# Kernel optimization log

Hardware: AMD Instinct MI355X
Metric: run time of the kernel (lower is better)

## Reference

```python
import jax, jax.numpy as jnp
import numpy as np

jax.config.update("jax_enable_x64", True)

B, T, D, L, H = 128, 256, 64, 64, 256   # batch, time steps, phys dim, latent dim, hidden width
P, DT = 4, 1.0                          # num_pred_steps, delta_t


def _mlp(x, ws, bs):
    # Conv1D(kernel_size=1) stack == per-timestep dense; relu hidden, linear output
    for i, (W, b) in enumerate(zip(ws, bs)):
        x = x @ W + b
        if i < len(ws) - 1:
            x = jax.nn.relu(x)
    return x


def setup_inputs() -> dict:
    key = jax.random.key(0)
    ks = jax.random.split(key, 9)

    def glorot(k, fi, fo):
        return jax.random.normal(k, (fi, fo), jnp.float64) * np.sqrt(2.0 / (fi + fo))

    inp = {"x": jax.random.normal(ks[0], (B, T, D), jnp.float64)}
    enc_dims = [(D, H), (H, H), (H, H), (H, L)]
    dec_dims = [(L, H), (H, H), (H, H), (H, D)]
    for i, (fi, fo) in enumerate(enc_dims):
        inp[f"enc_w{i}"] = glorot(ks[1 + i], fi, fo)
        inp[f"enc_b{i}"] = jnp.zeros((fo,), jnp.float64)
    for i, (fi, fo) in enumerate(dec_dims):
        inp[f"dec_w{i}"] = glorot(ks[5 + i], fi, fo)
        inp[f"dec_b{i}"] = jnp.zeros((fo,), jnp.float64)
    return inp


def _edmd(y, x):
    # y: [B, L, T] latent trajectories, x: [B, D, T] physical trajectories (D == L)
    y_m, y_p = y[:, :, :-1], y[:, :, 1:]
    # full_matrices=True followed by slicing to r=min(L,T-1)=L cols == reduced SVD
    U, S, Vh = jnp.linalg.svd(y_m, full_matrices=False)
    V = jnp.swapaxes(Vh, -1, -2)
    pinv = (V / S[:, None, :]) @ jnp.swapaxes(U, -1, -2)   # V @ diag(1/S) @ U^H
    K = y_p @ pinv                                         # [B, L, L]
    evals, modes = jnp.linalg.eig(K)                       # complex128
    k_evals = jnp.log(evals) / DT                          # [B, L]
    k_efuns = jnp.linalg.solve(modes, x.astype(modes.dtype))  # [B, L, T]
    xint = k_efuns[:, :, -1:]                              # [B, L, 1]

    # repeated squaring of diag eigenvalue matrix, one matvec per prediction step
    def step(e, _):
        yp = (modes @ (e[:, :, None] * xint))[..., 0]      # [B, L]
        return e * e, yp

    _, ys = jax.lax.scan(step, k_evals * k_evals, None, length=P)
    y_pred = jnp.transpose(ys, (1, 0, 2))                  # [B, P, L]
    return k_efuns, k_evals, modes, y_pred


def reference(x, enc_w0, enc_b0, enc_w1, enc_b1, enc_w2, enc_b2, enc_w3, enc_b3,
              dec_w0, dec_b0, dec_w1, dec_b1, dec_w2, dec_b2, dec_w3, dec_b3):
    ews = [enc_w0, enc_w1, enc_w2, enc_w3]
    ebs = [enc_b0, enc_b1, enc_b2, enc_b3]
    dws = [dec_w0, dec_w1, dec_w2, dec_w3]
    dbs = [dec_b0, dec_b1, dec_b2, dec_b3]

    y = _mlp(x, ews, ebs)        # [B, T, L]
    x_ae = _mlp(y, dws, dbs)     # [B, T, D]

    yt = jnp.swapaxes(y, 1, 2)   # [B, L, T]
    xt = jnp.swapaxes(x, 1, 2)   # [B, D, T]
    k_efuns, k_evals, k_modes, y_adv = _edmd(yt, xt)
    y_adv_real = jnp.real(y_adv)
    y_adv_imag = jnp.imag(y_adv)
    x_adv = _mlp(y_adv_real, dws, dbs)  # [B, P, D]
    return y, x_ae, x_adv, y_adv_real, y_adv_imag, k_evals, k_efuns, k_modes
```

## Files before the change

kernel.cpp:

```cpp
#include <hip/hip_runtime.h>
#include <hip/hip_bf16.h>

#define NB 128
#define NT 256
#define ND 64
#define NL 64
#define NH 256
#define NP 4

__device__ double g_ws[3932160];

static __device__ __forceinline__ double dlapy2_(double x, double y) {
  double ax = fabs(x), ay = fabs(y);
  double w = ax > ay ? ax : ay;
  double z = ax > ay ? ay : ax;
  if (z == 0.0) return w;
  double r = z / w;
  return w * sqrt(1.0 + r * r);
}
static __device__ __forceinline__ double sgn1_(double x) { return copysign(1.0, x); }
static __device__ __forceinline__ void cdiv_(double ar, double ai, double br, double bi,
                                             double& cr, double& ci) {
  if (fabs(br) >= fabs(bi)) {
    double r = bi / br, den = br + r * bi;
    cr = (ar + ai * r) / den;
    ci = (ai - ar * r) / den;
  } else {
    double r = br / bi, den = bi + r * br;
    cr = (ar * r + ai) / den;
    ci = (ai * r - ar) / den;
  }
}
static __device__ __forceinline__ void fwg(float* out, long long ofs, long long lim,
                                           double v) {
  if (ofs >= 0 && ofs < lim) out[ofs] = (float)v;
}
static __device__ __forceinline__ double wsum_(double v) {
  for (int o = 32; o > 0; o >>= 1) v += __shfl_xor(v, o, 64);
  return v;
}
static __device__ __forceinline__ double wmax_(double v) {
  for (int o = 32; o > 0; o >>= 1) v = fmax(v, __shfl_xor(v, o, 64));
  return v;
}
static __device__ __forceinline__ void wbar() {
  asm volatile("" ::: "memory");
  __builtin_amdgcn_wave_barrier();
  asm volatile("" ::: "memory");
}

static __device__ void dlanv2_(double& a, double& b, double& c, double& d,
                               double& rt1r, double& rt1i, double& rt2r, double& rt2i,
                               double& cs, double& sn) {
  const double eps = 2.2204460492503131e-16;
  if (c == 0.0) {
    cs = 1.0; sn = 0.0;
  } else if (b == 0.0) {
    cs = 0.0; sn = 1.0;
    double temp = d; d = a; a = temp;
    b = -c; c = 0.0;
  } else if ((a - d) == 0.0 && sgn1_(b) != sgn1_(c)) {
    cs = 1.0; sn = 0.0;
  } else {
    double temp = a - d;
    double p = 0.5 * temp;
    double bcmax = fmax(fabs(b), fabs(c));
    double bcmis = fmin(fabs(b), fabs(c)) * sgn1_(b) * sgn1_(c);
    double scale = fmax(fabs(p), bcmax);
    double z = (p / scale) * p + (bcmax / scale) * bcmis;
    if (z >= 4.0 * eps) {
      z = p + copysign(sqrt(scale) * sqrt(z), p);
      a = d + z;
      d = d - (bcmax / z) * bcmis;
      double tau = dlapy2_(c, z);
      cs = z / tau; sn = c / tau;
      b = b - c; c = 0.0;
    } else {
      double sigma = b + c;
      double tau = dlapy2_(sigma, temp);
      cs = sqrt(0.5 * (1.0 + fabs(sigma) / tau));
      sn = -(p / (tau * cs)) * sgn1_(sigma);
      double aa = a * cs + b * sn, bb = -a * sn + b * cs;
      double cc = c * cs + d * sn, dd = -c * sn + d * cs;
      a = aa * cs + cc * sn; b = bb * cs + dd * sn;
      c = -aa * sn + cc * cs; d = -bb * sn + dd * cs;
      temp = 0.5 * (a + d);
      a = temp; d = temp;
      if (c != 0.0) {
        if (b != 0.0) {
          if (sgn1_(b) == sgn1_(c)) {
            double sab = sqrt(fabs(b)), sac = sqrt(fabs(c));
            double p2 = copysign(sab * sac, c);
            double tau2 = 1.0 / sqrt(fabs(b + c));
            a = temp + p2; d = temp - p2;
            b = b - c; c = 0.0;
            double cs1 = sab * tau2, sn1 = sac * tau2;
            double t0 = cs * cs1 - sn * sn1;
            sn = cs * sn1 + sn * cs1;
            cs = t0;
          }
        } else {
          b = -c; c = 0.0;
          double t0 = cs; cs = -sn; sn = t0;
        }
      }
    }
  }
  rt1r = a; rt2r = d;
  if (c == 0.0) { rt1i = 0.0; rt2i = 0.0; }
  else { rt1i = sqrt(fabs(b)) * sqrt(fabs(c)); rt2i = -rt1i; }
}

__global__ __launch_bounds__(256) void enc_kernel(
    const float* __restrict__ x,
    const float* __restrict__ EW0, const float* __restrict__ EB0,
    const float* __restrict__ EW1, const float* __restrict__ EB1,
    const float* __restrict__ EW2, const float* __restrict__ EB2,
    const float* __restrict__ EW3, const float* __restrict__ EB3,
    float* __restrict__ out_y, double* __restrict__ y64, long long lim)
{
  const int tid = threadIdx.x;
  const long long tok0 = (long long)blockIdx.x * 8;
  __shared__ double xin[8][64];
  __shared__ double h0[8][256];
  __shared__ double h1[8][256];
  for (int idx = tid; idx < 512; idx += 256) {
    int tk = idx >> 6, f2 = idx & 63;
    xin[tk][f2] = (double)x[(tok0 + tk) * 64 + f2];
  }
  __syncthreads();
  {
    int j = tid; double acc[8]; double bj = (double)EB0[j];
    for (int tk = 0; tk < 8; ++tk) acc[tk] = bj;
#pragma unroll 8
    for (int i2 = 0; i2 < 64; ++i2) {
      double w = (double)EW0[i2 * 256 + j];
      for (int tk = 0; tk < 8; ++tk) acc[tk] += xin[tk][i2] * w;
    }
    for (int tk = 0; tk < 8; ++tk) h0[tk][j] = fmax(acc[tk], 0.0);
  }
  __syncthreads();
  {
    int j = tid; double acc[8]; double bj = (double)EB1[j];
    for (int tk = 0; tk < 8; ++tk) acc[tk] = bj;
#pragma unroll 4
    for (int i2 = 0; i2 < 256; ++i2) {
      double w = (double)EW1[i2 * 256 + j];
      for (int tk = 0; tk < 8; ++tk) acc[tk] += h0[tk][i2] * w;
    }
    for (int tk = 0; tk < 8; ++tk) h1[tk][j] = fmax(acc[tk], 0.0);
  }
  __syncthreads();
  {
    int j = tid; double acc[8]; double bj = (double)EB2[j];
    for (int tk = 0; tk < 8; ++tk) acc[tk] = bj;
#pragma unroll 4
    for (int i2 = 0; i2 < 256; ++i2) {
      double w = (double)EW2[i2 * 256 + j];
      for (int tk = 0; tk < 8; ++tk) acc[tk] += h1[tk][i2] * w;
    }
    for (int tk = 0; tk < 8; ++tk) h0[tk][j] = fmax(acc[tk], 0.0);
  }
  __syncthreads();
  {
    int j = tid & 63;
    int tg = tid >> 6;
    double acc0 = (double)EB3[j], acc1 = acc0;
#pragma unroll 4
    for (int i2 = 0; i2 < 256; ++i2) {
      double w = (double)EW3[i2 * 64 + j];
      acc0 += h0[tg * 2][i2] * w;
      acc1 += h0[tg * 2 + 1][i2] * w;
    }
    for (int u = 0; u < 2; ++u) {
      int tk = tg * 2 + u;
      double a = (u == 0) ? acc0 : acc1;
      long long gl = (tok0 + tk) * 64 + j;
      fwg(out_y, gl, lim, a);
      y64[gl] = a;
    }
  }
}

__global__ __launch_bounds__(256) void dec4_kernel(
    const double* __restrict__ inp, long long ntok,
    const float* __restrict__ W0, const float* __restrict__ B0,
    const float* __restrict__ W1, const float* __restrict__ B1,
    const float* __restrict__ W2, const float* __restrict__ B2,
    const float* __restrict__ W3, const float* __restrict__ B3,
    float* __restrict__ outb, long long lim)
{
  const int tid = threadIdx.x;
  const long long tok0 = (long long)blockIdx.x * 8;
  __shared__ double xin[8][64];
  __shared__ double h0[8][256];
  __shared__ double h1[8][256];
  for (int idx = tid; idx < 512; idx += 256) {
    int tk = idx >> 6, f2 = idx & 63;
    long long gl = (tok0 + tk) * 64 + f2;
    xin[tk][f2] = (tok0 + tk < ntok) ? inp[gl] : 0.0;
  }
  __syncthreads();
  {
    int j = tid; double acc[8]; double bj = (double)B0[j];
    for (int tk = 0; tk < 8; ++tk) acc[tk] = bj;
#pragma unroll 8
    for (int i2 = 0; i2 < 64; ++i2) {
      double w = (double)W0[i2 * 256 + j];
      for (int tk = 0; tk < 8; ++tk) acc[tk] += xin[tk][i2] * w;
    }
    for (int tk = 0; tk < 8; ++tk) h0[tk][j] = fmax(acc[tk], 0.0);
  }
  __syncthreads();
  {
    int j = tid; double acc[8]; double bj = (double)B1[j];
    for (int tk = 0; tk < 8; ++tk) acc[tk] = bj;
#pragma unroll 4
    for (int i2 = 0; i2 < 256; ++i2) {
      double w = (double)W1[i2 * 256 + j];
      for (int tk = 0; tk < 8; ++tk) acc[tk] += h0[tk][i2] * w;
    }
    for (int tk = 0; tk < 8; ++tk) h1[tk][j] = fmax(acc[tk], 0.0);
  }
  __syncthreads();
  {
    int j = tid; double acc[8]; double bj = (double)B2[j];
    for (int tk = 0; tk < 8; ++tk) acc[tk] = bj;
#pragma unroll 4
    for (int i2 = 0; i2 < 256; ++i2) {
      double w = (double)W2[i2 * 256 + j];
      for (int tk = 0; tk < 8; ++tk) acc[tk] += h1[tk][i2] * w;
    }
    for (int tk = 0; tk < 8; ++tk) h0[tk][j] = fmax(acc[tk], 0.0);
  }
  __syncthreads();
  {
    int j = tid & 63;
    int tg = tid >> 6;
    double acc0 = (double)B3[j], acc1 = acc0;
#pragma unroll 4
    for (int i2 = 0; i2 < 256; ++i2) {
      double w = (double)W3[i2 * 64 + j];
      acc0 += h0[tg * 2][i2] * w;
      acc1 += h0[tg * 2 + 1][i2] * w;
    }
    for (int u = 0; u < 2; ++u) {
      long long tok = tok0 + tg * 2 + u;
      if (tok < ntok) fwg(outb, tok * 64 + j, lim, (u == 0) ? acc0 : acc1);
    }
  }
}

__global__ __launch_bounds__(256) void buildGA_kernel(const double* __restrict__ y64,
                                                      double* __restrict__ G,
                                                      double* __restrict__ A)
{
  int b = blockIdx.x, tid = threadIdx.x;
  __shared__ double ybuf[65][64];
  const double* yb = y64 + (size_t)b * NT * 64;
  double g[16], a[16];
  for (int s = 0; s < 16; ++s) { g[s] = 0.0; a[s] = 0.0; }
  for (int c0 = 0; c0 < 255; c0 += 64) {
    int nrow = (256 - c0 < 65) ? (256 - c0) : 65;
    for (int idx = tid; idx < nrow * 64; idx += 256) {
      int rr = idx >> 6, f2 = idx & 63;
      ybuf[rr][f2] = yb[(size_t)(c0 + rr) * 64 + f2];
    }
    __syncthreads();
    int tmax = (254 - c0 < 63) ? (254 - c0) : 63;
    for (int s = 0; s < 16; ++s) {
      int id = s * 256 + tid;
      int i2 = id >> 6, j2 = id & 63;
      double gg = g[s], aa = a[s];
      for (int tt = 0; tt <= tmax; ++tt) {
        double yj = ybuf[tt][j2];
        gg += ybuf[tt][i2] * yj;
        aa += ybuf[tt + 1][i2] * yj;
      }
      g[s] = gg; a[s] = aa;
    }
    __syncthreads();
  }
  for (int s = 0; s < 16; ++s) {
    int id = s * 256 + tid;
    G[(size_t)b * 4096 + id] = g[s];
    A[(size_t)b * 4096 + id] = a[s];
  }
}

__global__ __launch_bounds__(64) void cholsolve_kernel(const double* __restrict__ G,
                                                       const double* __restrict__ A,
                                                       double* __restrict__ Km)
{
  int b = blockIdx.x, t = threadIdx.x;
  __shared__ double C[64][65];
  __shared__ double X[64][65];
  const double* Gb = G + (size_t)b * 4096;
  const double* Ab = A + (size_t)b * 4096;
  for (int r = 0; r < 64; ++r) C[r][t] = Gb[r * 64 + t];
  for (int i2 = 0; i2 < 64; ++i2) X[i2][t] = Ab[t * 64 + i2];
  __syncthreads();
  for (int k = 0; k < 64; ++k) {
    double s = C[k][k];
    for (int m2 = 0; m2 < k; ++m2) s -= C[k][m2] * C[k][m2];
    double ckk = sqrt(fmax(s, 1e-300));
    wbar();
    if (t == k) C[k][k] = ckk;
    if (t > k) {
      double v = C[t][k];
      for (int m2 = 0; m2 < k; ++m2) v -= C[t][m2] * C[k][m2];
      C[t][k] = v / ckk;
    }
    wbar();
  }
  for (int i2 = 0; i2 < 64; ++i2) {
    double v = X[i2][t];
    for (int m2 = 0; m2 < i2; ++m2) v -= C[i2][m2] * X[m2][t];
    X[i2][t] = v / C[i2][i2];
  }
  for (int i2 = 63; i2 >= 0; --i2) {
    double v = X[i2][t];
    for (int m2 = i2 + 1; m2 < 64; ++m2) v -= C[m2][i2] * X[m2][t];
    X[i2][t] = v / C[i2][i2];
  }
  wbar();
  for (int i2 = 0; i2 < 64; ++i2)
    Km[(size_t)b * 4096 + (size_t)t * 64 + i2] = X[i2][t];
}

__global__ __launch_bounds__(64) void eig_dec_kernel(
    const double* __restrict__ Kmat,
    double* __restrict__ modes_re, double* __restrict__ modes_im,
    double* __restrict__ klog,
    float* __restrict__ out, long long o_kevals, long long o_kmodes,
    int cplx, long long lim,
    const double* __restrict__ y64,
    const float* __restrict__ DW0, const float* __restrict__ DB0,
    const float* __restrict__ DW1, const float* __restrict__ DB1,
    const float* __restrict__ DW2, const float* __restrict__ DB2,
    const float* __restrict__ DW3, const float* __restrict__ DB3,
    float* __restrict__ out_xae)
{
  const int t = threadIdx.x;
  __shared__ __align__(16) double smem[8704];

  if (blockIdx.x >= NB) {
    const int blk = blockIdx.x - NB;
    const long long tok0 = (long long)blk * 8;
    float (*fx)[64] = (float (*)[64])(smem);
    float (*fh0)[256] = (float (*)[256])(smem + 256);
    float (*fh1)[256] = (float (*)[256])(smem + 1280);
    for (int idx = t; idx < 512; idx += 64) {
      int tk = idx >> 6, f2 = idx & 63;
      fx[tk][f2] = (float)y64[(tok0 + tk) * 64 + f2];
    }
    __syncthreads();
    float acc[4][8];
    for (int s = 0; s < 4; ++s) {
      float bj = DB0[t + 64 * s];
      for (int tk = 0; tk < 8; ++tk) acc[s][tk] = bj;
    }
#pragma unroll 4
    for (int i = 0; i < 64; ++i) {
      float xv[8];
      for (int tk = 0; tk < 8; ++tk) xv[tk] = fx[tk][i];
      for (int s = 0; s < 4; ++s) {
        float w = DW0[i * 256 + t + 64 * s];
        for (int tk = 0; tk < 8; ++tk) acc[s][tk] += xv[tk] * w;
      }
    }
    for (int s = 0; s < 4; ++s)
      for (int tk = 0; tk < 8; ++tk) fh0[tk][t + 64 * s] = fmaxf(acc[s][tk], 0.0f);
    __syncthreads();
    for (int s = 0; s < 4; ++s) {
      float bj = DB1[t + 64 * s];
      for (int tk = 0; tk < 8; ++tk) acc[s][tk] = bj;
    }
#pragma unroll 2
    for (int i = 0; i < 256; ++i) {
      float xv[8];
      for (int tk = 0; tk < 8; ++tk) xv[tk] = fh0[tk][i];
      for (int s = 0; s < 4; ++s) {
        float w = DW1[i * 256 + t + 64 * s];
        for (int tk = 0; tk < 8; ++tk) acc[s][tk] += xv[tk] * w;
      }
    }
    for (int s = 0; s < 4; ++s)
      for (int tk = 0; tk < 8; ++tk) fh1[tk][t + 64 * s] = fmaxf(acc[s][tk], 0.0f);
    __syncthreads();
    for (int s = 0; s < 4; ++s) {
      float bj = DB2[t + 64 * s];
      for (int tk = 0; tk < 8; ++tk) acc[s][tk] = bj;
    }
#pragma unroll 2
    for (int i = 0; i < 256; ++i) {
      float xv[8];
      for (int tk = 0; tk < 8; ++tk) xv[tk] = fh1[tk][i];
      for (int s = 0; s < 4; ++s) {
        float w = DW2[i * 256 + t + 64 * s];
        for (int tk = 0; tk < 8; ++tk) acc[s][tk] += xv[tk] * w;
      }
    }
    for (int s = 0; s < 4; ++s)
      for (int tk = 0; tk < 8; ++tk) fh0[tk][t + 64 * s] = fmaxf(acc[s][tk], 0.0f);
    __syncthreads();
    float a4[8];
    float bj3 = DB3[t];
    for (int tk = 0; tk < 8; ++tk) a4[tk] = bj3;
#pragma unroll 2
    for (int i = 0; i < 256; ++i) {
      float w = DW3[i * 64 + t];
      for (int tk = 0; tk < 8; ++tk) a4[tk] += fh0[tk][i] * w;
    }
    for (int tk = 0; tk < 8; ++tk)
      fwg(out_xae, (tok0 + tk) * 64 + t, lim, (double)a4[tk]);
    return;
  }

  const int b = blockIdx.x;
  double (*Hs)[65] = (double (*)[65])smem;
  double (*Zs)[65] = (double (*)[65])(smem + 4160);
  double* wr = smem + 8320;
  double* wi = wr + 64;
  double* bscale = wi + 64;
  double* tau = bscale + 64;
  double* xr = tau + 64;
  double* xi = xr + 64;
  double* mre = modes_re + (size_t)b * 4096;
  double* mim = modes_im + (size_t)b * 4096;

  const double ulp = 2.2204460492503131e-16;
  const double safmin = 2.2250738585072014e-308;

  for (int r = 0; r < 64; ++r) Hs[r][t] = Kmat[(size_t)b * 4096 + r * 64 + t];
  bscale[t] = 1.0;
  __syncthreads();

  {
    const double sclfac = 2.0, factor = 0.95;
    const double sfmin1 = safmin / ulp;
    const double sfmax1 = 1.0 / sfmin1;
    const double sfmin2 = sfmin1 * sclfac;
    const double sfmax2 = 1.0 / sfmin2;
    for (int sweep = 0; sweep < 64; ++sweep) {
      bool noconv = false;
      for (int i = 0; i < 64; ++i) {
        double colv = fabs(Hs[t][i]);
        double rowv = fabs(Hs[i][t]);
        double c = wsum_((t == i) ? 0.0 : colv);
        double r = wsum_((t == i) ? 0.0 : rowv);
        double ca = wmax_(colv);
        double ra = wmax_(rowv);
        if (c == 0.0 || r == 0.0) continue;
        double g = r / sclfac, f = 1.0, s = c + r;
        while (c < g) {
          if (fmax(fmax(f, c), ca) >= sfmax2 || fmin(fmin(r, g), ra) <= sfmin2) break;
          f *= sclfac; c *= sclfac; ca *= sclfac;
          r /= sclfac; g /= sclfac; ra /= sclfac;
        }
        g = c / sclfac;
        while (g >= r) {
          if (fmax(r, ra) >= sfmax2 || fmin(fmin(fmin(f, c), g), ca) <= sfmin2) break;
          f /= sclfac; c /= sclfac; g /= sclfac; ca /= sclfac;
          r *= sclfac; ra *= sclfac;
        }
        if (c + r >= factor * s) continue;
        double bsi = bscale[i];
        if (f < 1.0 && bsi < 1.0) { if (f * bsi <= sfmin1) continue; }
        if (f > 1.0 && bsi > 1.0) { if (bsi >= sfmax1 / f) continue; }
        double gi = 1.0 / f;
        Hs[i][t] *= gi;
        Hs[t][i] *= f;
        if (t == 0) bscale[i] = bsi * f;
        noconv = true;
        wbar();
      }
      if (!noconv) break;
    }
    wbar();
  }

  for (int i = 0; i < 62; ++i) {
    double alpha = Hs[i + 1][i];
    double contrib = (t >= i + 2) ? Hs[t][i] * Hs[t][i] : 0.0;
    double ss = wsum_(contrib);
    double taui, beta;
    if (ss == 0.0) {
      taui = 0.0; beta = alpha;
    } else {
      beta = -copysign(sqrt(alpha * alpha + ss), alpha);
      taui = (beta - alpha) / beta;
      double sc = 1.0 / (alpha - beta);
      if (t >= i + 2) Hs[t][i] *= sc;
    }
    if (t == 0) { tau[i] = taui; Hs[i + 1][i] = beta; }
    wbar();
    if (taui != 0.0) {
      {
        double sum = Hs[t][i + 1];
        for (int k = i + 2; k < 64; ++k) sum += Hs[t][k] * Hs[k][i];
        sum *= taui;
        Hs[t][i + 1] -= sum;
        for (int k = i + 2; k < 64; ++k) Hs[t][k] -= sum * Hs[k][i];
      }
      wbar();
      if (t >= i + 1) {
        double sum = Hs[i + 1][t];
        for (int k = i + 2; k < 64; ++k) sum += Hs[k][i] * Hs[k][t];
        sum *= taui;
        Hs[i + 1][t] -= sum;
        for (int k = i + 2; k < 64; ++k) Hs[k][t] -= sum * Hs[k][i];
      }
      wbar();
    }
  }

  {
    for (int r = 0; r < 64; ++r) Zs[t][r] = (r == t) ? 1.0 : 0.0;
    for (int i = 61; i >= 0; --i) {
      double taui = tau[i];
      if (taui != 0.0) {
        double sum = Zs[t][i + 1];
        for (int k = i + 2; k < 64; ++k) sum += Hs[k][i] * Zs[t][k];
        sum *= taui;
        Zs[t][i + 1] -= sum;
        for (int k = i + 2; k < 64; ++k) Zs[t][k] -= sum * Hs[k][i];
      }
    }
  }
  wbar();
  for (int r = t + 2; r < 64; ++r) Hs[r][t] = 0.0;
  __syncthreads();

  {
    const int lo = 0, hi = 63;
    const double dat1 = 0.75, dat2 = -0.4375;
    const int kexsh = 10;
    const double smlnum = safmin * (64.0 / ulp);
    int I = hi;
    int kdefl = 0;
    while (I >= lo) {
      int L = lo;
      bool done = false;
      const int itmax = 30 * 64;
      for (int its = 0; its <= itmax; ++its) {
        int k;
        {
          bool pred = false;
          int kl = t;
          if (kl > L && kl <= I) {
            double sub = fabs(Hs[kl][kl - 1]);
            if (sub <= smlnum) pred = true;
            else {
              double tst = fabs(Hs[kl - 1][kl - 1]) + fabs(Hs[kl][kl]);
              if (tst == 0.0) {
                if (kl - 2 >= lo) tst += fabs(Hs[kl - 1][kl - 2]);
                if (kl + 1 <= hi) tst += fabs(Hs[kl + 1][kl]);
              }
              if (sub <= ulp * tst) {
                double h12a = fabs(Hs[kl - 1][kl]);
                double ab = fmax(sub, h12a), ba = fmin(sub, h12a);
                double hkk = fabs(Hs[kl][kl]);
                double dif = fabs(Hs[kl - 1][kl - 1] - Hs[kl][kl]);
                double aa = fmax(hkk, dif), bb2 = fmin(hkk, dif);
                double s = aa + ab;
                if (ba * (ab / s) <= fmax(smlnum, ulp * (bb2 * (aa / s)))) pred = true;
              }
            }
          }
          unsigned long long msk = __ballot(pred);
          k = msk ? (63 - __builtin_clzll(msk)) : L;
        }
        L = k;
        if (L > lo) { if (t == 0) Hs[L][L - 1] = 0.0; }
        wbar();
        if (L >= I - 1) { done = true; break; }
        kdefl++;
        double h11, h12, h21, h22;
        if (kdefl % (2 * kexsh) == 0) {
          double s = dat1 * (fabs(Hs[I][I - 1]) + fabs(Hs[I - 1][I - 2]));
          h11 = dat2 * s + Hs[I][I]; h12 = s; h21 = s; h22 = h11;
        } else if (kdefl % kexsh == 0) {
          double s = dat1 * (fabs(Hs[L + 1][L]) + fabs(Hs[L + 2][L + 1]));
          h11 = dat2 * s + Hs[L][L]; h12 = s; h21 = s; h22 = h11;
        } else {
          h11 = Hs[I - 1][I - 1]; h21 = Hs[I][I - 1];
          h12 = Hs[I - 1][I];     h22 = Hs[I][I];
        }
        double rt1r, rt1i, rt2r, rt2i;
        {
          double s = fabs(h11) + fabs(h12) + fabs(h21) + fabs(h22);
          if (s == 0.0) { rt1r = rt1i = rt2r = rt2i = 0.0; }
          else {
            double a_ = h11 / s, c_ = h21 / s, b_ = h12 / s, d_ = h22 / s;
            double tr = a_ + d_;
            double det = (a_ - d_) * (a_ - d_) * 0.25 + b_ * c_;
            if (det >= 0.0) {
              double rtdisc = sqrt(det);
              double r1 = tr * 0.5 + rtdisc;
              double r2 = tr * 0.5 - rtdisc;
              double pick = (fabs(r1 - d_) <= fabs(r2 - d_)) ? r1 : r2;
              rt1r = pick * s; rt2r = rt1r; rt1i = 0.0; rt2i = 0.0;
            } else {
              rt1r = tr * 0.5 * s; rt2r = rt1r;
              rt1i = sqrt(-det) * s; rt2i = -rt1i;
            }
          }
        }
        int m; double v0, v1, v2;
        {
          double w0 = 0.0, w1 = 0.0, w2 = 0.0;
          bool ok = false;
          int mm = t;
          if (mm >= L && mm <= I - 2) {
            double h21s = Hs[mm + 1][mm];
            double s = fabs(Hs[mm][mm] - rt2r) + fabs(rt2i) + fabs(h21s);
            h21s = Hs[mm + 1][mm] / s;
            w0 = h21s * Hs[mm][mm + 1] + (Hs[mm][mm] - rt1r) * ((Hs[mm][mm] - rt2r) / s)
                 - rt1i * (rt2i / s);
            w1 = h21s * (Hs[mm][mm] + Hs[mm + 1][mm + 1] - rt1r - rt2r);
            w2 = h21s * Hs[mm + 2][mm + 1];
            double s2 = fabs(w0) + fabs(w1) + fabs(w2);
            w0 /= s2; w1 /= s2; w2 /= s2;
            if (mm == L) ok = true;
            else ok = (fabs(Hs[mm][mm - 1]) * (fabs(w1) + fabs(w2)) <=
                       ulp * fabs(w0) *
                           (fabs(Hs[mm - 1][mm - 1]) + fabs(Hs[mm][mm]) +
                            fabs(Hs[mm + 1][mm + 1])));
          }
          unsigned long long msk = __ballot(ok);
          m = 63 - __builtin_clzll(msk);
          v0 = __shfl(w0, m); v1 = __shfl(w1, m); v2 = __shfl(w2, m);
        }
        double c0 = 0.0, c1 = 0.0, c2 = 0.0;
        double zc0 = 0.0, zc1 = 0.0;
        for (int kk = m; kk <= I - 1; ++kk) {
          int nr = (3 < I - kk + 1) ? 3 : (I - kk + 1);
          double a0 = Hs[kk][t];
          double a1 = Hs[kk + 1][t];
          double a2 = (nr == 3) ? Hs[kk + 2][t] : 0.0;
          double z0, z1;
          if (kk > m) { z0 = zc0; z1 = zc1; }
          else { z0 = Zs[kk][t]; z1 = Zs[kk + 1][t]; }
          double z2 = (nr == 3) ? Zs[kk + 2][t] : 0.0;
          double u0, u1, u2 = 0.0;
          if (kk > m) { u0 = c0; u1 = c1; u2 = (nr == 3) ? c2 : 0.0; }
          else        { u0 = v0; u1 = v1; u2 = (nr == 3) ? v2 : 0.0; }
          double t1;
          {
            double xn2 = u1 * u1 + u2 * u2;
            if (xn2 == 0.0) t1 = 0.0;
            else {
              double beta = -copysign(sqrt(u0 * u0 + xn2), u0);
              t1 = (beta - u0) / beta;
              double sc = 1.0 / (u0 - beta);
              u1 *= sc; u2 *= sc;
              u0 = beta;
            }
          }
          double t2 = t1 * u1, t3 = t1 * u2;
          if (t >= kk) {
            double sum = a0 + u1 * a1 + u2 * a2;
            Hs[kk][t] = a0 - sum * t1;
            Hs[kk + 1][t] = a1 - sum * t2;
            if (nr == 3) Hs[kk + 2][t] = a2 - sum * t3;
          }
          if (t == 0) {
            if (kk > m) {
              Hs[kk][kk - 1] = u0;
              Hs[kk + 1][kk - 1] = 0.0;
              if (kk < I - 1) Hs[kk + 2][kk - 1] = 0.0;
            } else if (m > L) {
              Hs[kk][kk - 1] *= (1.0 - t1);
            }
          }
          wbar();
          int rmax = (kk + 3 < I) ? kk + 3 : I;
          double nv0 = 0.0;
          if (t <= rmax) {
            double b0 = Hs[t][kk], b1 = Hs[t][kk + 1];
            double b2 = (nr == 3) ? Hs[t][kk + 2] : 0.0;
            double sB = b0 + u1 * b1 + u2 * b2;
            nv0 = b0 - sB * t1;
            Hs[t][kk] = nv0;
            Hs[t][kk + 1] = b1 - sB * t2;
            if (nr == 3) Hs[t][kk + 2] = b2 - sB * t3;
          }
          {
            double sZ = z0 + u1 * z1 + u2 * z2;
            Zs[kk][t] = z0 - sZ * t1;
            zc0 = z1 - sZ * t2;
            Zs[kk + 1][t] = zc0;
            if (nr == 3) {
              zc1 = z2 - sZ * t3;
              Zs[kk + 2][t] = zc1;
            }
          }
          int s1 = (kk + 1 < 64) ? kk + 1 : 63;
          int s2 = (kk + 2 < 64) ? kk + 2 : 63;
          int s3 = (kk + 3 < 64) ? kk + 3 : 63;
          c0 = __shfl(nv0, s1, 64);
          c1 = __shfl(nv0, s2, 64);
          c2 = __shfl(nv0, s3, 64);
          wbar();
        }
      }
      if (!done) {
        wbar();
        if (t == 0) {
          for (int r = lo; r <= I; ++r) { wr[r] = Hs[r][r]; wi[r] = 0.0; }
        }
        wbar();
        I = lo - 1;
        kdefl = 0;
        continue;
      }
      if (L == I) {
        if (t == 0) { wr[I] = Hs[I][I]; wi[I] = 0.0; }
        wbar();
      } else {
        double a_ = Hs[I - 1][I - 1], b_ = Hs[I - 1][I];
        double c_ = Hs[I][I - 1],     d_ = Hs[I][I];
        double r1r, r1i, r2r, r2i, cs, sn;
        dlanv2_(a_, b_, c_, d_, r1r, r1i, r2r, r2i, cs, sn);
        wbar();
        if (t == 0) {
          Hs[I - 1][I - 1] = a_; Hs[I - 1][I] = b_;
          Hs[I][I - 1] = c_;     Hs[I][I] = d_;
          wr[I - 1] = r1r; wi[I - 1] = r1i;
          wr[I] = r2r;     wi[I] = r2i;
        }
        wbar();
        if (t > I) {
          double x = Hs[I - 1][t], y = Hs[I][t];
          Hs[I - 1][t] = cs * x + sn * y;
          Hs[I][t] = cs * y - sn * x;
        }
        if (t < I - 1) {
          double x = Hs[t][I - 1], y = Hs[t][I];
          Hs[t][I - 1] = cs * x + sn * y;
          Hs[t][I] = cs * y - sn * x;
        }
        {
          double x = Zs[I - 1][t], y = Zs[I][t];
          Zs[I - 1][t] = cs * x + sn * y;
          Zs[I][t] = cs * y - sn * x;
        }
        wbar();
      }
      kdefl = 0;
      I = L - 1;
    }
  }
  __syncthreads();

  const double smln = safmin * (64.0 / ulp);
  int ki = 63;
  while (ki >= 0) {
    wbar();
    bool pair = (ki > 0) && (Hs[ki][ki - 1] != 0.0);
    if (!pair) {
      double lam = wr[ki];
      double smin = fmax(ulp * fabs(lam), smln);
      xr[t] = (t < ki) ? -Hs[t][ki] : ((t == ki) ? 1.0 : 0.0);
      wbar();
      int j = ki - 1;
      while (j >= 0) {
        bool blk2 = (j > 0) && (Hs[j][j - 1] != 0.0);
        if (!blk2) {
          double den = Hs[j][j] - lam;
          if (fabs(den) < smin) den = smin;
          double xj = xr[j] / den;
          if (t == j) xr[j] = xj;
          else if (t < j) xr[t] -= xj * Hs[t][j];
          wbar();
          j -= 1;
        } else {
          double t11 = Hs[j - 1][j - 1] - lam, t12 = Hs[j - 1][j];
          double t21 = Hs[j][j - 1], t22 = Hs[j][j] - lam;
          double det = t11 * t22 - t12 * t21;
          if (fabs(det) < smin * smin) det = copysign(smin * smin, (det == 0.0) ? 1.0 : det);
          double b1 = xr[j - 1], b2 = xr[j];
          double x1 = (b1 * t22 - t12 * b2) / det;
          double x2 = (t11 * b2 - t21 * b1) / det;
          if (t == j - 1) xr[j - 1] = x1;
          else if (t == j) xr[j] = x2;
          else if (t < j - 1) xr[t] -= x1 * Hs[t][j - 1] + x2 * Hs[t][j];
          wbar();
          j -= 2;
        }
      }
      double acc = 0.0;
      for (int k2 = 0; k2 <= ki; ++k2) acc += Zs[k2][t] * xr[k2];
      acc *= bscale[t];
      double nn = wsum_(acc * acc);
      double scl = 1.0 / sqrt(nn);
      mre[t * 64 + ki] = acc * scl;
      mim[t * 64 + ki] = 0.0;
      ki -= 1;
    } else {
      double wre = Hs[ki][ki];
      double wim = sqrt(fabs(Hs[ki][ki - 1])) * sqrt(fabs(Hs[ki - 1][ki]));
      double smin = fmax(ulp * (fabs(wre) + wim), smln);
      double seed_r_km1, seed_i_k;
      if (fabs(Hs[ki - 1][ki]) >= fabs(Hs[ki][ki - 1])) {
        seed_r_km1 = 1.0;
        seed_i_k = wim / Hs[ki - 1][ki];
      } else {
        seed_r_km1 = -wim / Hs[ki][ki - 1];
        seed_i_k = 1.0;
      }
      if (t < ki - 1) {
        xr[t] = -seed_r_km1 * Hs[t][ki - 1];
        xi[t] = -seed_i_k * Hs[t][ki];
      } else if (t == ki - 1) { xr[t] = seed_r_km1; xi[t] = 0.0; }
      else if (t == ki) { xr[t] = 0.0; xi[t] = seed_i_k; }
      else { xr[t] = 0.0; xi[t] = 0.0; }
      wbar();
      int j = ki - 2;
      while (j >= 0) {
        bool blk2 = (j > 0) && (Hs[j][j - 1] != 0.0);
        if (!blk2) {
          double dr = Hs[j][j] - wre, di = -wim;
          if (fabs(dr) + fabs(di) < smin) { dr = smin; di = 0.0; }
          double xjr, xji;
          cdiv_(xr[j], xi[j], dr, di, xjr, xji);
          if (t == j) { xr[j] = xjr; xi[j] = xji; }
          else if (t < j) {
            xr[t] -= xjr * Hs[t][j];
            xi[t] -= xji * Hs[t][j];
          }
          wbar();
          j -= 1;
        } else {
          double t11 = Hs[j - 1][j - 1] - wre, t12 = Hs[j - 1][j];
          double t21 = Hs[j][j - 1], t22 = Hs[j][j] - wre;
          double detr = t11 * t22 - wim * wim - t12 * t21;
          double deti = -wim * (t11 + t22);
          double b1r = xr[j - 1], b1i = xi[j - 1];
          double b2r = xr[j], b2i = xi[j];
          double n1r = b1r * t22 + b1i * wim - t12 * b2r;
          double n1i = b1i * t22 - b1r * wim - t12 * b2i;
          double n2r = t11 * b2r + b2i * wim - t21 * b1r;
          double n2i = t11 * b2i - b2r * wim - t21 * b1i;
          double x1r, x1i, x2r, x2i;
          cdiv_(n1r, n1i, detr, deti, x1r, x1i);
          cdiv_(n2r, n2i, detr, deti, x2r, x2i);
          if (t == j - 1) { xr[t] = x1r; xi[t] = x1i; }
          else if (t == j) { xr[t] = x2r; xi[t] = x2i; }
          else if (t < j - 1) {
            xr[t] -= x1r * Hs[t][j - 1] + x2r * Hs[t][j];
            xi[t] -= x1i * Hs[t][j - 1] + x2i * Hs[t][j];
          }
          wbar();
          j -= 2;
        }
      }
      double ar = 0.0, ai = 0.0;
      for (int k2 = 0; k2 <= ki; ++k2) {
        double z = Zs[k2][t];
        ar += z * xr[k2];
        ai += z * xi[k2];
      }
      ar *= bscale[t]; ai *= bscale[t];
      double n2a = wsum_(ar * ar), n2b = wsum_(ai * ai);
      double scl = 1.0 / dlapy2_(sqrt(n2a), sqrt(n2b));
      double vr0 = ar * scl, vi0 = ai * scl;
      double mm = vr0 * vr0 + vi0 * vi0;
      double mmax = wmax_(mm);
      unsigned long long msk = __ballot(mm == mmax);
      int kmx = __ffsll((unsigned long long)msk) - 1;
      double f = __shfl(vr0, kmx), g = __shfl(vi0, kmx);
      double cs_, sn_;
      if (g == 0.0) { cs_ = 1.0; sn_ = 0.0; }
      else if (f == 0.0) { cs_ = 0.0; sn_ = sgn1_(g); }
      else {
        double dd = sqrt(f * f + g * g);
        double sg = sgn1_(f);
        cs_ = fabs(f) / dd;
        sn_ = sg * g / dd;
      }
      double nr0 = cs_ * vr0 + sn_ * vi0;
      double ni0 = cs_ * vi0 - sn_ * vr0;
      if (t == kmx) ni0 = 0.0;
      mre[t * 64 + (ki - 1)] = nr0;
      mim[t * 64 + (ki - 1)] = ni0;
      mre[t * 64 + ki] = nr0;
      mim[t * 64 + ki] = -ni0;
      ki -= 2;
    }
  }

  {
    double er = wr[t], ei = wi[t];
    double lr = log(dlapy2_(er, ei));
    double li = atan2(ei, er);
    klog[(size_t)b * 128 + 2 * t] = lr;
    klog[(size_t)b * 128 + 2 * t + 1] = li;
    if (cplx) {
      fwg(out, o_kevals + ((long long)b * 64 + t) * 2, lim, lr);
      fwg(out, o_kevals + ((long long)b * 64 + t) * 2 + 1, lim, li);
    } else {
      fwg(out, o_kevals + (long long)b * 64 + t, lim, lr);
    }
  }
  for (int k2 = 0; k2 < 64; ++k2) {
    long long idx = ((long long)b * 64 + t) * 64 + k2;
    if (cplx) {
      fwg(out, o_kmodes + idx * 2, lim, mre[t * 64 + k2]);
      fwg(out, o_kmodes + idx * 2 + 1, lim, mim[t * 64 + k2]);
    } else {
      fwg(out, o_kmodes + idx, lim, mre[t * 64 + k2]);
    }
  }
}

__global__ __launch_bounds__(64) void lu_kernel(
    const double* __restrict__ mre, const double* __restrict__ mim,
    double* __restrict__ lure, double* __restrict__ luim, int* __restrict__ piv)
{
  int b = blockIdx.x, t = threadIdx.x;
  __shared__ double Lre[64][65], Lim[64][65];
  for (int r = 0; r < 64; ++r) {
    Lre[r][t] = mre[(size_t)b * 4096 + r * 64 + t];
    Lim[r][t] = mim[(size_t)b * 4096 + r * 64 + t];
  }
  __syncthreads();
  for (int k = 0; k < 64; ++k) {
    double mval = (t >= k) ? (fabs(Lre[t][k]) + fabs(Lim[t][k])) : -1.0;
    double mmax = wmax_(mval);
    unsigned long long msk = __ballot(mval == mmax);
    int p = __ffsll(msk) - 1;
    if (t == 0) piv[b * 64 + k] = p;
    if (p != k) {
      double a0 = Lre[k][t], a1 = Lim[k][t];
      Lre[k][t] = Lre[p][t]; Lim[k][t] = Lim[p][t];
      Lre[p][t] = a0; Lim[p][t] = a1;
    }
    wbar();
    double pr = Lre[k][k], pi = Lim[k][k];
    if (t > k) {
      double lr, li;
      cdiv_(Lre[t][k], Lim[t][k], pr, pi, lr, li);
      Lre[t][k] = lr; Lim[t][k] = li;
      for (int c = k + 1; c < 64; ++c) {
        double ur = Lre[k][c], ui = Lim[k][c];
        Lre[t][c] -= lr * ur - li * ui;
        Lim[t][c] -= lr * ui + li * ur;
      }
    }
    wbar();
  }
  for (int r = 0; r < 64; ++r) {
    lure[(size_t)b * 4096 + r * 64 + t] = Lre[r][t];
    luim[(size_t)b * 4096 + r * 64 + t] = Lim[r][t];
  }
}

__global__ __launch_bounds__(64) void lusolve_kernel(
    const double* __restrict__ lure, const double* __restrict__ luim,
    const int* __restrict__ piv, const float* __restrict__ x_in,
    float* __restrict__ out, long long o_kefuns, int cplx,
    double* __restrict__ xint, long long lim)
{
  int b = blockIdx.x >> 2;
  int chunk = blockIdx.x & 3;
  int t = threadIdx.x;
  int tglob = chunk * 64 + t;
  __shared__ double br_[64][64], bi_[64][64];
  const double* Lr = lure + (size_t)b * 4096;
  const double* Li = luim + (size_t)b * 4096;
  for (int i2 = 0; i2 < 64; ++i2) {
    br_[i2][t] = (double)x_in[((size_t)b * 256 + tglob) * 64 + i2];
    bi_[i2][t] = 0.0;
  }
  const int* pv = piv + b * 64;
  for (int k = 0; k < 64; ++k) {
    int p = pv[k];
    if (p != k) {
      double a0 = br_[k][t], a1 = bi_[k][t];
      br_[k][t] = br_[p][t]; bi_[k][t] = bi_[p][t];
      br_[p][t] = a0; bi_[p][t] = a1;
    }
  }
  for (int k = 0; k < 63; ++k) {
    double bkr = br_[k][t], bki = bi_[k][t];
    for (int i2 = k + 1; i2 < 64; ++i2) {
      double lr = Lr[i2 * 64 + k], li = Li[i2 * 64 + k];
      br_[i2][t] -= lr * bkr - li * bki;
      bi_[i2][t] -= lr * bki + li * bkr;
    }
  }
  for (int k = 63; k >= 0; --k) {
    double xr0, xi0;
    cdiv_(br_[k][t], bi_[k][t], Lr[k * 64 + k], Li[k * 64 + k], xr0, xi0);
    br_[k][t] = xr0; bi_[k][t] = xi0;
    for (int i2 = 0; i2 < k; ++i2) {
      double ur = Lr[i2 * 64 + k], ui = Li[i2 * 64 + k];
      br_[i2][t] -= ur * xr0 - ui * xi0;
      bi_[i2][t] -= ur * xi0 + ui * xr0;
    }
  }
  for (int i2 = 0; i2 < 64; ++i2) {
    long long idx = ((long long)b * 64 + i2) * 256 + tglob;
    if (cplx) {
      fwg(out, o_kefuns + idx * 2, lim, br_[i2][t]);
      fwg(out, o_kefuns + idx * 2 + 1, lim, bi_[i2][t]);
    } else {
      fwg(out, o_kefuns + idx, lim, br_[i2][t]);
    }
  }
  if (tglob == 255) {
    for (int i2 = 0; i2 < 64; ++i2) {
      xint[(size_t)b * 128 + 2 * i2] = br_[i2][t];
      xint[(size_t)b * 128 + 2 * i2 + 1] = bi_[i2][t];
    }
  }
}

__global__ __launch_bounds__(64) void ypred_kernel(
    const double* __restrict__ klog, const double* __restrict__ xint,
    const double* __restrict__ mre, const double* __restrict__ mim,
    float* __restrict__ out, long long o_yadvr, long long o_yadvi,
    double* __restrict__ yadv64, long long lim)
{
  int b = blockIdx.x, t = threadIdx.x;
  __shared__ double er[64], ei[64], wxr[64], wxi[64];
  double kr = klog[(size_t)b * 128 + 2 * t], kiv = klog[(size_t)b * 128 + 2 * t + 1];
  er[t] = kr * kr - kiv * kiv;
  ei[t] = 2.0 * kr * kiv;
  double xr0 = xint[(size_t)b * 128 + 2 * t], xi0 = xint[(size_t)b * 128 + 2 * t + 1];
  __syncthreads();
  for (int p = 0; p < 4; ++p) {
    wxr[t] = er[t] * xr0 - ei[t] * xi0;
    wxi[t] = er[t] * xi0 + ei[t] * xr0;
    __syncthreads();
    double ar = 0.0, ai = 0.0;
    const double* mr = mre + (size_t)b * 4096 + (size_t)t * 64;
    const double* mi = mim + (size_t)b * 4096 + (size_t)t * 64;
    for (int k = 0; k < 64; ++k) {
      double wr0 = wxr[k], wi0 = wxi[k];
      ar += mr[k] * wr0 - mi[k] * wi0;
      ai += mr[k] * wi0 + mi[k] * wr0;
    }
    long long idx = ((long long)b * 4 + p) * 64 + t;
    fwg(out, o_yadvr + idx, lim, ar);
    fwg(out, o_yadvi + idx, lim, ai);
    yadv64[idx] = ar;
    double e2r = er[t] * er[t] - ei[t] * ei[t];
    double e2i = 2.0 * er[t] * ei[t];
    __syncthreads();
    er[t] = e2r; ei[t] = e2i;
    __syncthreads();
  }
}

extern "C" void kernel_launch(void* const* d_in, const int* in_sizes, int n_in,
                              void* d_out, int out_size, void* d_ws, size_t ws_size,
                              hipStream_t stream) {
  (void)in_sizes; (void)n_in; (void)d_ws; (void)ws_size;
  const float* x = (const float*)d_in[0];
  const float* ew0 = (const float*)d_in[1];  const float* eb0 = (const float*)d_in[2];
  const float* ew1 = (const float*)d_in[3];  const float* eb1 = (const float*)d_in[4];
  const float* ew2 = (const float*)d_in[5];  const float* eb2 = (const float*)d_in[6];
  const float* ew3 = (const float*)d_in[7];  const float* eb3 = (const float*)d_in[8];
  const float* dw0 = (const float*)d_in[9];  const float* db0 = (const float*)d_in[10];
  const float* dw1 = (const float*)d_in[11]; const float* db1 = (const float*)d_in[12];
  const float* dw2 = (const float*)d_in[13]; const float* db2 = (const float*)d_in[14];
  const float* dw3 = (const float*)d_in[15]; const float* db3 = (const float*)d_in[16];
  float* out = (float*)d_out;
  const long long lim = (long long)out_size;

  void* wsp = nullptr;
  hipGetSymbolAddress(&wsp, HIP_SYMBOL(g_ws));
  char* ws = (char*)wsp;
  double* y64  = (double*)(ws + 0);
  double* G    = (double*)(ws + 16777216);
  double* A    = (double*)(ws + 20971520);
  double* Km   = (double*)(ws + 25165824);
  double* mre  = (double*)(ws + 16777216);
  double* mim  = (double*)(ws + 20971520);
  double* lure = (double*)(ws + 25165824);
  double* luim = (double*)(ws + 0);
  double* klog = (double*)(ws + 29360128);
  double* xint = (double*)(ws + 29491200);
  double* yadv = (double*)(ws + 29622272);
  int*    piv  = (int*)   (ws + 29884416);

  const long long n_y = 2097152, n_s = 32768;
  int cplx = (out_size > 8000000) ? 1 : 0;
  long long o_y = 0, o_xae = n_y, o_xadv = 2 * n_y;
  long long o_yadvr = o_xadv + n_s, o_yadvi = o_yadvr + n_s;
  long long o_kevals = o_yadvi + n_s;
  long long o_kefuns, o_kmodes;
  if (cplx) { o_kefuns = o_kevals + 2 * 8192;  o_kmodes = o_kefuns + 2 * 2097152; }
  else      { o_kefuns = o_kevals + 8192;      o_kmodes = o_kefuns + 2097152; }

  enc_kernel<<<4096, 256, 0, stream>>>(x,
      ew0, eb0, ew1, eb1, ew2, eb2, ew3, eb3, out + o_y, y64, lim);
  buildGA_kernel<<<128, 256, 0, stream>>>(y64, G, A);
  cholsolve_kernel<<<128, 64, 0, stream>>>(G, A, Km);
  eig_dec_kernel<<<128 + 4096, 64, 0, stream>>>(Km, mre, mim, klog,
      out, o_kevals, o_kmodes, cplx, lim,
      y64, dw0, db0, dw1, db1, dw2, db2, dw3, db3, out + o_xae);
  lu_kernel<<<128, 64, 0, stream>>>(mre, mim, lure, luim, piv);
  lusolve_kernel<<<512, 64, 0, stream>>>(lure, luim, piv, x, out, o_kefuns, cplx,
                                         xint, lim);
  ypred_kernel<<<128, 64, 0, stream>>>(klog, xint, mre, mim, out, o_yadvr, o_yadvi,
                                       yadv, lim);
  dec4_kernel<<<64, 256, 0, stream>>>(yadv, 512,
      dw0, db0, dw1, db1, dw2, db2, dw3, db3, out + o_xadv, lim);
}
```

Before: 4.652 ms.

## Compute next bulge Householder vector speculatively and use fast reciprocals in QR sweep

In the Francis double-shift QR bulge-chase loop, the next iteration's Householder vector is now computed before the wave barrier. It applies the row and column reflections to the needed entries redundantly through shuffles, removing the post-update shuffle chain from the serial critical path. Double-precision divisions are replaced by a float reciprocal refined with two Newton iterations. This adds redundant shuffles and arithmetic per step and may change rounding slightly relative to exact division.

```diff
diff --git a/kernel.cpp b/kernel.cpp
--- a/kernel.cpp
+++ b/kernel.cpp
@@ -34,6 +34,14 @@
 static __device__ __forceinline__ void fwg(float* out, long long ofs, long long lim,
                                            double v) {
   if (ofs >= 0 && ofs < lim) out[ofs] = (float)v;
+}
+static __device__ __forceinline__ double frcp_(double d) {
+  float df = (float)d;
+  if (df == 0.0f || !isfinite(df)) return 1.0 / d;
+  double r = (double)(1.0f / df);
+  r = r * (2.0 - d * r);
+  r = r * (2.0 - d * r);
+  return r;
 }
 static __device__ __forceinline__ double wsum_(double v) {
   for (int o = 32; o > 0; o >>= 1) v += __shfl_xor(v, o, 64);
@@ -632,38 +640,44 @@
           m = 63 - __builtin_clzll(msk);
           v0 = __shfl(w0, m); v1 = __shfl(w1, m); v2 = __shfl(w2, m);
         }
-        double c0 = 0.0, c1 = 0.0, c2 = 0.0;
+        double nu0 = 0.0, nu1 = 0.0, nu2 = 0.0;
         double zc0 = 0.0, zc1 = 0.0;
         for (int kk = m; kk <= I - 1; ++kk) {
           int nr = (3 < I - kk + 1) ? 3 : (I - kk + 1);
           double a0 = Hs[kk][t];
           double a1 = Hs[kk + 1][t];
           double a2 = (nr == 3) ? Hs[kk + 2][t] : 0.0;
+          double p0 = Hs[t][kk];
+          double p1 = Hs[t][kk + 1];
+          double p2 = (nr == 3) ? Hs[t][kk + 2] : 0.0;
           double z0, z1;
           if (kk > m) { z0 = zc0; z1 = zc1; }
           else { z0 = Zs[kk][t]; z1 = Zs[kk + 1][t]; }
           double z2 = (nr == 3) ? Zs[kk + 2][t] : 0.0;
           double u0, u1, u2 = 0.0;
-          if (kk > m) { u0 = c0; u1 = c1; u2 = (nr == 3) ? c2 : 0.0; }
-          else        { u0 = v0; u1 = v1; u2 = (nr == 3) ? v2 : 0.0; }
+          if (kk > m) { u0 = nu0; u1 = nu1; u2 = (nr == 3) ? nu2 : 0.0; }
+          else        { u0 = v0;  u1 = v1;  u2 = (nr == 3) ? v2 : 0.0; }
           double t1;
           {
             double xn2 = u1 * u1 + u2 * u2;
             if (xn2 == 0.0) t1 = 0.0;
             else {
               double beta = -copysign(sqrt(u0 * u0 + xn2), u0);
-              t1 = (beta - u0) / beta;
-              double sc = 1.0 / (u0 - beta);
+              t1 = (beta - u0) * frcp_(beta);
+              double sc = frcp_(u0 - beta);
               u1 *= sc; u2 *= sc;
               u0 = beta;
             }
           }
           double t2 = t1 * u1, t3 = t1 * u2;
+          double sA = a0 + u1 * a1 + u2 * a2;
+          double n0 = a0 - sA * t1;
+          double n1 = a1 - sA * t2;
+          double n2 = a2 - sA * t3;
           if (t >= kk) {
-            double sum = a0 + u1 * a1 + u2 * a2;
-            Hs[kk][t] = a0 - sum * t1;
-            Hs[kk + 1][t] = a1 - sum * t2;
-            if (nr == 3) Hs[kk + 2][t] = a2 - sum * t3;
+            Hs[kk][t] = n0;
+            Hs[kk + 1][t] = n1;
+            if (nr == 3) Hs[kk + 2][t] = n2;
           }
           if (t == 0) {
             if (kk > m) {
@@ -674,15 +688,25 @@
               Hs[kk][kk - 1] *= (1.0 - t1);
             }
           }
+          {
+            int sk2 = (kk + 2 < 64) ? kk + 2 : 63;
+            int sk3 = (kk + 3 < 64) ? kk + 3 : 63;
+            double prevw = p0 - (p0 + u1 * p1 + u2 * p2) * t1;
+            double n1a = __shfl(n1, kk, 64), n1b = __shfl(n1, kk + 1, 64),
+                   n1c = __shfl(n1, sk2, 64);
+            double n2a = __shfl(n2, kk, 64), n2b = __shfl(n2, kk + 1, 64),
+                   n2c = __shfl(n2, sk2, 64);
+            nu0 = n1a - (n1a + u1 * n1b + u2 * n1c) * t1;
+            nu1 = n2a - (n2a + u1 * n2b + u2 * n2c) * t1;
+            nu2 = __shfl(prevw, sk3, 64);
+          }
           wbar();
           int rmax = (kk + 3 < I) ? kk + 3 : I;
-          double nv0 = 0.0;
           if (t <= rmax) {
             double b0 = Hs[t][kk], b1 = Hs[t][kk + 1];
             double b2 = (nr == 3) ? Hs[t][kk + 2] : 0.0;
             double sB = b0 + u1 * b1 + u2 * b2;
-            nv0 = b0 - sB * t1;
-            Hs[t][kk] = nv0;
+            Hs[t][kk] = b0 - sB * t1;
             Hs[t][kk + 1] = b1 - sB * t2;
             if (nr == 3) Hs[t][kk + 2] = b2 - sB * t3;
           }
@@ -696,12 +720,6 @@
               Zs[kk + 2][t] = zc1;
             }
           }
-          int s1 = (kk + 1 < 64) ? kk + 1 : 63;
-          int s2 = (kk + 2 < 64) ? kk + 2 : 63;
-          int s3 = (kk + 3 < 64) ? kk + 3 : 63;
-          c0 = __shfl(nv0, s1, 64);
-          c1 = __shfl(nv0, s2, 64);
-          c2 = __shfl(nv0, s3, 64);
           wbar();
         }
       }
```

Measured after the change: 5.442 ms. 1.17x slower.
